# Kernel tuning notes

Measured on AMD Instinct MI355X. Metric: run time of the kernel, lower is better.

## Reference

```python
import jax, jax.numpy as jnp
import numpy as np

KH = KW = 3
C_IN = 3
FILTERS = 32
STRIDE = 2
LN_EPS = 1e-3  # keras LayerNormalization default


def _conv(inp, k, strides):
    return jax.lax.conv_general_dilated(
        inp, k, window_strides=strides, padding='SAME',
        dimension_numbers=('NHWC', 'HWIO', 'NHWC'))


def _hard_sigmoid(z):
    # keras hard_sigmoid: 0.2*x + 0.5, clipped to [0, 1]
    return jnp.clip(z * 0.2 + 0.5, 0.0, 1.0)


def setup_inputs() -> dict:
    key = jax.random.key(0)
    ks = jax.random.split(key, 6)
    B, T, H, W = 16, 24, 112, 112
    F = FILTERS
    Hp, Wp = H // STRIDE, W // STRIDE
    D = Hp * Wp * F
    x = jax.random.normal(ks[0], (B, T, H, W, C_IN), dtype=jnp.float32)
    Wk = jax.random.normal(ks[1], (KH, KW, C_IN, 4 * F), dtype=jnp.float32) * 0.05
    Uk = jax.random.normal(ks[2], (KH, KW, F, 4 * F), dtype=jnp.float32) * 0.05
    b = jax.random.normal(ks[3], (4 * F,), dtype=jnp.float32) * 0.05
    gamma = jnp.ones((D,), dtype=jnp.float32)
    beta = jnp.zeros((D,), dtype=jnp.float32)
    return {'x': x, 'Wk': Wk, 'Uk': Uk, 'b': b, 'gamma': gamma, 'beta': beta}


def reference(x, Wk, Uk, b, gamma, beta):
    B, T, H, W, C = x.shape
    F = Uk.shape[2]
    # Input-to-gate convs are time-independent: batch them over B*T in one conv.
    xg = _conv(x.reshape(B * T, H, W, C), Wk, (STRIDE, STRIDE)) + b
    Hp, Wp = xg.shape[1], xg.shape[2]
    xg = xg.reshape(B, T, Hp, Wp, 4 * F).transpose(1, 0, 2, 3, 4)  # (T,B,Hp,Wp,4F)

    def step(carry, xt):
        h, c = carry
        z = xt + _conv(h, Uk, (1, 1))
        zi, zf, zc, zo = jnp.split(z, 4, axis=-1)
        i = _hard_sigmoid(zi)
        f = _hard_sigmoid(zf)
        o = _hard_sigmoid(zo)
        c_new = f * c + i * jnp.tanh(zc)
        h_new = o * jnp.tanh(c_new)
        return (h_new, c_new), h_new

    h0 = jnp.zeros((B, Hp, Wp, F), x.dtype)
    _, hs = jax.lax.scan(step, (h0, h0), xg)  # hs: (T,B,Hp,Wp,F)

    y = hs.transpose(1, 0, 2, 3, 4).reshape(B, T, Hp * Wp * F)
    mu = jnp.mean(y, axis=-1, keepdims=True)
    var = jnp.mean(jnp.square(y - mu), axis=-1, keepdims=True)
    yn = (y - mu) * jax.lax.rsqrt(var + LN_EPS)
    return yn * gamma + beta
```

## Files before the change

kernel.cpp:

```cpp
#include <hip/hip_runtime.h>
#include <math.h>

#define NB 16
#define NT 24
#define HP 56
#define WP 56
#define NF 32
#define ND (HP*WP*NF)
#define NHPQ 14
#define HPITCH 36
#define LN_EPS 1e-3f

typedef __attribute__((ext_vector_type(8))) short short8;
typedef __attribute__((ext_vector_type(4))) float floatx4;

#define AT_LD(p)     __hip_atomic_load((p), __ATOMIC_RELAXED, __HIP_MEMORY_SCOPE_AGENT)
#define AT_ST(p, v)  __hip_atomic_store((p), (v), __ATOMIC_RELAXED, __HIP_MEMORY_SCOPE_AGENT)
#define AT_ADD(p, v) __hip_atomic_fetch_add((p), (v), __ATOMIC_RELAXED, __HIP_MEMORY_SCOPE_AGENT)

__device__ __forceinline__ float tanh_fast(float x){
    float e = __expf(2.0f*x);
    return 1.0f - 2.0f*__builtin_amdgcn_rcpf(e + 1.0f);
}
__device__ __forceinline__ float hsig(float z){
    return fminf(fmaxf(z*0.2f + 0.5f, 0.0f), 1.0f);
}
__device__ __forceinline__ ushort f2bf(float v){
    unsigned u = __float_as_uint(v);
    return (ushort)((u + 0x7fffu + ((u >> 16) & 1u)) >> 16);
}

__global__ __launch_bounds__(512, 2)
void convlstm_persist(const float* __restrict__ x,
                      const float* __restrict__ Wk,
                      const float* __restrict__ Uk,
                      const float* __restrict__ bias,
                      const float* __restrict__ gamma,
                      const float* __restrict__ beta,
                      ushort* __restrict__ hbuf0,
                      ushort* __restrict__ hbuf1,
                      float* __restrict__ out,
                      float* __restrict__ stats,
                      int* __restrict__ cnt,
                      int* __restrict__ flags)
{
    __shared__ __attribute__((aligned(16))) ushort h_lds[6*66*HPITCH];
    __shared__ __attribute__((aligned(16))) ushort x_lds[9*344];
    __shared__ __attribute__((aligned(16))) ushort u_lds[9*128*32];
    __shared__ __attribute__((aligned(16))) ushort wk_lds[128*32];
    __shared__ float bcast[2];
    __shared__ float sred[8][2];

    const int tid  = threadIdx.x;
    const int hpq  = blockIdx.x;
    const int b    = blockIdx.y;
    const int lane = tid & 63;
    const int w    = tid >> 6;
    const int row  = w >> 1;
    const int fh   = w & 1;
    const int col  = lane & 15;
    const int q    = lane >> 4;
    const int q8   = q * 8;
    const int hp_g = hpq*4 + row;

    for (int e = tid; e < 6*66*HPITCH; e += 512) h_lds[e] = 0;
    for (int e = tid; e < 9*344;       e += 512) x_lds[e] = 0;
    for (int e = tid; e < 9*32*128; e += 512){
        int tap = e >> 12, k = (e >> 7) & 31, n = e & 127;
        u_lds[(tap*128 + n)*32 + k] = f2bf(Uk[e]);
    }
    for (int e = tid; e < 128*32; e += 512){
        int n = e >> 5, k = e & 31;
        wk_lds[e] = (k < 27) ? f2bf(Wk[k*128 + n]) : (ushort)0;
    }

    float bg[4];
    #pragma unroll
    for (int g = 0; g < 4; g++) bg[g] = bias[g*32 + fh*16 + col];

    float gr[4][4], br[4][4], creg[4][4], hreg[4][4];
    #pragma unroll
    for (int mt = 0; mt < 4; mt++)
      #pragma unroll
      for (int reg = 0; reg < 4; reg++){
          int wp = mt*16 + q*4 + reg;
          creg[mt][reg] = 0.f;
          hreg[mt][reg] = 0.f;
          if (wp < WP){
              size_t idx = (size_t)(hp_g*WP + wp)*NF + fh*16 + col;
              gr[mt][reg] = gamma[idx];
              br[mt][reg] = beta[idx];
          } else { gr[mt][reg] = 0.f; br[mt][reg] = 0.f; }
      }

    __syncthreads();

    for (int t = 0; t < NT; ++t){
        {
            const float* xt = x + ((size_t)(b*NT + t))*(112*112*3);
            for (int e = tid; e < 9*84; e += 512){
                int rrow = e / 84;
                int c4   = e - rrow*84;
                int rg   = 8*hpq + rrow;
                if (rg < 112){
                    float4 v = *(const float4*)&xt[rg*336 + c4*4];
                    ushort4 s4 = {f2bf(v.x), f2bf(v.y), f2bf(v.z), f2bf(v.w)};
                    *(ushort4*)&x_lds[rrow*344 + c4*4] = s4;
                }
            }
        }
        if (t > 0 && tid == 0){
            const int fb = ((t-1)*NB + b)*NHPQ;
            if (hpq > 0)
                while (AT_LD(&flags[fb + hpq-1]) == 0) __builtin_amdgcn_s_sleep(4);
            if (hpq < NHPQ-1)
                while (AT_LD(&flags[fb + hpq+1]) == 0) __builtin_amdgcn_s_sleep(4);
            asm volatile("" ::: "memory");
        }
        __syncthreads();

        uint4 hv = {0u,0u,0u,0u};
        int hoff = -1;
        if (t > 0 && tid < 448){
            const ushort* hsrc = ((t & 1) ? hbuf0 : hbuf1) + (size_t)b*ND;
            int rsel = (tid >= 224);
            int rem  = tid - rsel*224;
            int cg   = rem >> 2, cq = rem & 3;
            int rg   = rsel ? (hpq*4 + 4) : (hpq*4 - 1);
            int ldr  = rsel ? 5 : 0;
            if (rg >= 0 && rg < HP){
                const uint* sp = (const uint*)&hsrc[((size_t)rg*WP + cg)*NF + cq*8];
                hv.x = AT_LD(sp + 0);
                hv.y = AT_LD(sp + 1);
                hv.z = AT_LD(sp + 2);
                hv.w = AT_LD(sp + 3);
                hoff = (ldr*66 + 1 + cg)*HPITCH + cq*8;
            }
        }

        floatx4 acc[4][4];
        #pragma unroll
        for (int g = 0; g < 4; g++){
            floatx4 bv = (floatx4){bg[g], bg[g], bg[g], bg[g]};
            #pragma unroll
            for (int mt = 0; mt < 4; mt++) acc[mt][g] = bv;
        }

        {
            short8 ax[4];
            #pragma unroll
            for (int mt = 0; mt < 4; mt++){
                int wp = mt*16 + col;
                short8 v;
                #pragma unroll
                for (int j = 0; j < 8; j++){
                    int k = q8 + j;
                    ushort bits = 0;
                    if (k < 27){
                        int dy = k/9; int rr = k - dy*9; int dx = rr/3; int cc = rr - dx*3;
                        int xc = 2*wp + dx; if (xc > 112) xc = 112;
                        bits = x_lds[(2*row + dy)*344 + xc*3 + cc];
                    }
                    v[j] = (short)bits;
                }
                ax[mt] = v;
            }
            #pragma unroll
            for (int g = 0; g < 4; g++){
                short8 bx = *(const short8*)&wk_lds[(g*32 + fh*16 + col)*32 + q8];
                #pragma unroll
                for (int mt = 0; mt < 4; mt++)
                    acc[mt][g] = __builtin_amdgcn_mfma_f32_16x16x32_bf16(ax[mt], bx, acc[mt][g], 0, 0, 0);
            }
        }

        if (hoff >= 0) *(uint4*)&h_lds[hoff] = hv;
        __syncthreads();

        if (t > 0){
            #pragma unroll
            for (int tap = 0; tap < 9; tap++){
                int dy = tap/3, dx = tap - dy*3;
                short8 a_[4], bb_[4];
                #pragma unroll
                for (int g = 0; g < 4; g++)
                    bb_[g] = *(const short8*)&u_lds[(tap*128 + g*32 + fh*16 + col)*32 + q8];
                #pragma unroll
                for (int mt = 0; mt < 4; mt++)
                    a_[mt] = *(const short8*)&h_lds[((row + dy)*66 + mt*16 + col + dx)*HPITCH + q8];
                #pragma unroll
                for (int mt = 0; mt < 4; mt++)
                    #pragma unroll
                    for (int g = 0; g < 4; g++)
                        acc[mt][g] = __builtin_amdgcn_mfma_f32_16x16x32_bf16(a_[mt], bb_[g], acc[mt][g], 0, 0, 0);
            }
        }
        __syncthreads();

        if (t > 0){
            if (tid == 0){
                while (AT_LD(&cnt[b*NT + t-1]) < NHPQ) __builtin_amdgcn_s_sleep(4);
                asm volatile("" ::: "memory");
                float s  = AT_LD(&stats[(size_t)(b*NT + t-1)*2]);
                float ss = AT_LD(&stats[(size_t)(b*NT + t-1)*2 + 1]);
                float m  = s * (1.0f/(float)ND);
                float v  = ss * (1.0f/(float)ND) - m*m;
                bcast[0] = m;
                bcast[1] = rsqrtf(v + LN_EPS);
            }
            __syncthreads();
            const float mu = bcast[0], rs = bcast[1];
            float* orow = out + ((size_t)(b*NT + t - 1))*ND;
            #pragma unroll
            for (int mt = 0; mt < 4; mt++)
              #pragma unroll
              for (int reg = 0; reg < 4; reg++){
                  int wp = mt*16 + q*4 + reg;
                  if (wp < WP)
                      orow[(size_t)(hp_g*WP + wp)*NF + fh*16 + col] =
                          (hreg[mt][reg] - mu)*rs*gr[mt][reg] + br[mt][reg];
              }
        }

        float lsum = 0.f, lss = 0.f;
        #pragma unroll
        for (int mt = 0; mt < 4; mt++)
          #pragma unroll
          for (int reg = 0; reg < 4; reg++){
              int wp = mt*16 + q*4 + reg;
              float zi = acc[mt][0][reg];
              float zf = acc[mt][1][reg];
              float zc = acc[mt][2][reg];
              float zo = acc[mt][3][reg];
              float ig = hsig(zi), fg = hsig(zf), og = hsig(zo);
              float cn = fg*creg[mt][reg] + ig*tanh_fast(zc);
              float hv2 = og*tanh_fast(cn);
              if (wp < WP){
                  creg[mt][reg] = cn;
                  hreg[mt][reg] = hv2;
                  h_lds[((row + 1)*66 + 1 + wp)*HPITCH + fh*16 + col] = f2bf(hv2);
                  lsum += hv2;
                  lss  += hv2*hv2;
              }
          }

        if (row == 0 || row == 3){
            ushort* hdst = ((t & 1) ? hbuf1 : hbuf0) + (size_t)b*ND;
            int rg  = hpq*4 + row;
            int ldr = row ? 4 : 1;
            for (int e = lane; e < 112; e += 64){
                int cg = e >> 1, hf = e & 1;
                uint4 v = *(const uint4*)&h_lds[(ldr*66 + 1 + cg)*HPITCH + fh*16 + hf*8];
                uint* dp = (uint*)&hdst[((size_t)rg*WP + cg)*NF + fh*16 + hf*8];
                AT_ST(dp + 0, v.x);
                AT_ST(dp + 1, v.y);
                AT_ST(dp + 2, v.z);
                AT_ST(dp + 3, v.w);
            }
        }

        #pragma unroll
        for (int off = 32; off > 0; off >>= 1){
            lsum += __shfl_down(lsum, off);
            lss  += __shfl_down(lss, off);
        }
        if (lane == 0){ sred[w][0] = lsum; sred[w][1] = lss; }

        asm volatile("s_waitcnt vmcnt(0)" ::: "memory");
        __syncthreads();
        if (tid == 0){
            float a0 = 0.f, a1 = 0.f;
            #pragma unroll
            for (int i = 0; i < 8; i++){ a0 += sred[i][0]; a1 += sred[i][1]; }
            AT_ADD(&stats[(size_t)(b*NT + t)*2],     a0);
            AT_ADD(&stats[(size_t)(b*NT + t)*2 + 1], a1);
            asm volatile("s_waitcnt vmcnt(0)" ::: "memory");
            AT_ADD(&cnt[b*NT + t], 1);
            AT_ADD(&flags[((size_t)t*NB + b)*NHPQ + hpq], 1);
        }
    }

    if (tid == 0){
        while (AT_LD(&cnt[b*NT + NT-1]) < NHPQ) __builtin_amdgcn_s_sleep(4);
        asm volatile("" ::: "memory");
        float s  = AT_LD(&stats[(size_t)(b*NT + NT-1)*2]);
        float ss = AT_LD(&stats[(size_t)(b*NT + NT-1)*2 + 1]);
        float m  = s * (1.0f/(float)ND);
        float v  = ss * (1.0f/(float)ND) - m*m;
        bcast[0] = m;
        bcast[1] = rsqrtf(v + LN_EPS);
    }
    __syncthreads();
    {
        const float mu = bcast[0], rs = bcast[1];
        float* orow = out + ((size_t)(b*NT + NT - 1))*ND;
        #pragma unroll
        for (int mt = 0; mt < 4; mt++)
          #pragma unroll
          for (int reg = 0; reg < 4; reg++){
              int wp = mt*16 + q*4 + reg;
              if (wp < WP)
                  orow[(size_t)(hp_g*WP + wp)*NF + fh*16 + col] =
                      (hreg[mt][reg] - mu)*rs*gr[mt][reg] + br[mt][reg];
          }
    }
}

extern "C" void kernel_launch(void* const* d_in, const int* in_sizes, int n_in,
                              void* d_out, int out_size, void* d_ws, size_t ws_size,
                              hipStream_t stream)
{
    const float* x     = (const float*)d_in[0];
    const float* Wk    = (const float*)d_in[1];
    const float* Uk    = (const float*)d_in[2];
    const float* bias  = (const float*)d_in[3];
    const float* gamma = (const float*)d_in[4];
    const float* beta  = (const float*)d_in[5];
    float* out = (float*)d_out;

    char* p = (char*)d_ws;
    ushort* hbuf0 = (ushort*)p; p += (size_t)NB*ND*2;
    ushort* hbuf1 = (ushort*)p; p += (size_t)NB*ND*2;
    float*  stats = (float*)p;  p += (size_t)NB*NT*2*4;
    int*    cnt   = (int*)p;    p += (size_t)NB*NT*4;
    int*    flags = (int*)p;

    hipMemsetAsync(stats, 0, (size_t)(NB*NT*2*4 + NB*NT*4 + NT*NB*NHPQ*4), stream);
    hipLaunchKernelGGL(convlstm_persist, dim3(NHPQ, NB), dim3(512), 0, stream,
                       x, Wk, Uk, bias, gamma, beta,
                       hbuf0, hbuf1, out, stats, cnt, flags);
}
```

Baseline: 571.3 us.

## Defer LayerNorm output by two steps and signal halo flags earlier

The LayerNorm write-out for each timestep is delayed by two steps, so the global stats wait overlaps with an extra step of recurrence. This keeps two generations of h in registers and raises register pressure. Halo-ready flags are now raised once the boundary-row warps finish their global stores, instead of after the full block reduction, using an LDS counter. The change also pads the weight LDS layout to pitch 36 to reduce bank conflicts and shortens the spin-wait sleep.

```diff
diff --git a/kernel.cpp b/kernel.cpp
--- a/kernel.cpp
+++ b/kernel.cpp
@@ -9,6 +9,7 @@
 #define ND (HP*WP*NF)
 #define NHPQ 14
 #define HPITCH 36
+#define UPITCH 36
 #define LN_EPS 1e-3f
 
 typedef __attribute__((ext_vector_type(8))) short short8;
@@ -46,10 +47,11 @@
 {
     __shared__ __attribute__((aligned(16))) ushort h_lds[6*66*HPITCH];
     __shared__ __attribute__((aligned(16))) ushort x_lds[9*344];
-    __shared__ __attribute__((aligned(16))) ushort u_lds[9*128*32];
-    __shared__ __attribute__((aligned(16))) ushort wk_lds[128*32];
-    __shared__ float bcast[2];
+    __shared__ __attribute__((aligned(16))) ushort u_lds[9*128*UPITCH];
+    __shared__ __attribute__((aligned(16))) ushort wk_lds[128*UPITCH];
+    __shared__ float bcast4[4];
     __shared__ float sred[8][2];
+    __shared__ int   ecnt[NT];
 
     const int tid  = threadIdx.x;
     const int hpq  = blockIdx.x;
@@ -67,25 +69,25 @@
     for (int e = tid; e < 9*344;       e += 512) x_lds[e] = 0;
     for (int e = tid; e < 9*32*128; e += 512){
         int tap = e >> 12, k = (e >> 7) & 31, n = e & 127;
-        u_lds[(tap*128 + n)*32 + k] = f2bf(Uk[e]);
+        u_lds[(tap*128 + n)*UPITCH + k] = f2bf(Uk[e]);
     }
     for (int e = tid; e < 128*32; e += 512){
         int n = e >> 5, k = e & 31;
-        wk_lds[e] = (k < 27) ? f2bf(Wk[k*128 + n]) : (ushort)0;
-    }
+        wk_lds[n*UPITCH + k] = (k < 27) ? f2bf(Wk[k*128 + n]) : (ushort)0;
+    }
+    for (int e = tid; e < NT; e += 512) ecnt[e] = 0;
 
     float bg[4];
     #pragma unroll
     for (int g = 0; g < 4; g++) bg[g] = bias[g*32 + fh*16 + col];
 
-    float gr[4][4], br[4][4], creg[4][4], hreg[4][4];
+    float gr[4][4], br[4][4], creg[4][4], hregA[4][4], hregB[4][4];
     #pragma unroll
     for (int mt = 0; mt < 4; mt++)
       #pragma unroll
       for (int reg = 0; reg < 4; reg++){
           int wp = mt*16 + q*4 + reg;
-          creg[mt][reg] = 0.f;
-          hreg[mt][reg] = 0.f;
+          creg[mt][reg] = 0.f; hregA[mt][reg] = 0.f; hregB[mt][reg] = 0.f;
           if (wp < WP){
               size_t idx = (size_t)(hp_g*WP + wp)*NF + fh*16 + col;
               gr[mt][reg] = gamma[idx];
@@ -112,9 +114,9 @@
         if (t > 0 && tid == 0){
             const int fb = ((t-1)*NB + b)*NHPQ;
             if (hpq > 0)
-                while (AT_LD(&flags[fb + hpq-1]) == 0) __builtin_amdgcn_s_sleep(4);
+                while (AT_LD(&flags[fb + hpq-1]) == 0) __builtin_amdgcn_s_sleep(1);
             if (hpq < NHPQ-1)
-                while (AT_LD(&flags[fb + hpq+1]) == 0) __builtin_amdgcn_s_sleep(4);
+                while (AT_LD(&flags[fb + hpq+1]) == 0) __builtin_amdgcn_s_sleep(1);
             asm volatile("" ::: "memory");
         }
         __syncthreads();
@@ -167,7 +169,7 @@
             }
             #pragma unroll
             for (int g = 0; g < 4; g++){
-                short8 bx = *(const short8*)&wk_lds[(g*32 + fh*16 + col)*32 + q8];
+                short8 bx = *(const short8*)&wk_lds[(g*32 + fh*16 + col)*UPITCH + q8];
                 #pragma unroll
                 for (int mt = 0; mt < 4; mt++)
                     acc[mt][g] = __builtin_amdgcn_mfma_f32_16x16x32_bf16(ax[mt], bx, acc[mt][g], 0, 0, 0);
@@ -184,7 +186,7 @@
                 short8 a_[4], bb_[4];
                 #pragma unroll
                 for (int g = 0; g < 4; g++)
-                    bb_[g] = *(const short8*)&u_lds[(tap*128 + g*32 + fh*16 + col)*32 + q8];
+                    bb_[g] = *(const short8*)&u_lds[(tap*128 + g*32 + fh*16 + col)*UPITCH + q8];
                 #pragma unroll
                 for (int mt = 0; mt < 4; mt++)
                     a_[mt] = *(const short8*)&h_lds[((row + dy)*66 + mt*16 + col + dx)*HPITCH + q8];
@@ -197,31 +199,7 @@
         }
         __syncthreads();
 
-        if (t > 0){
-            if (tid == 0){
-                while (AT_LD(&cnt[b*NT + t-1]) < NHPQ) __builtin_amdgcn_s_sleep(4);
-                asm volatile("" ::: "memory");
-                float s  = AT_LD(&stats[(size_t)(b*NT + t-1)*2]);
-                float ss = AT_LD(&stats[(size_t)(b*NT + t-1)*2 + 1]);
-                float m  = s * (1.0f/(float)ND);
-                float v  = ss * (1.0f/(float)ND) - m*m;
-                bcast[0] = m;
-                bcast[1] = rsqrtf(v + LN_EPS);
-            }
-            __syncthreads();
-            const float mu = bcast[0], rs = bcast[1];
-            float* orow = out + ((size_t)(b*NT + t - 1))*ND;
-            #pragma unroll
-            for (int mt = 0; mt < 4; mt++)
-              #pragma unroll
-              for (int reg = 0; reg < 4; reg++){
-                  int wp = mt*16 + q*4 + reg;
-                  if (wp < WP)
-                      orow[(size_t)(hp_g*WP + wp)*NF + fh*16 + col] =
-                          (hreg[mt][reg] - mu)*rs*gr[mt][reg] + br[mt][reg];
-              }
-        }
-
+        float hnew[4][4];
         float lsum = 0.f, lss = 0.f;
         #pragma unroll
         for (int mt = 0; mt < 4; mt++)
@@ -235,9 +213,10 @@
               float ig = hsig(zi), fg = hsig(zf), og = hsig(zo);
               float cn = fg*creg[mt][reg] + ig*tanh_fast(zc);
               float hv2 = og*tanh_fast(cn);
+              hnew[mt][reg] = 0.f;
               if (wp < WP){
                   creg[mt][reg] = cn;
-                  hreg[mt][reg] = hv2;
+                  hnew[mt][reg] = hv2;
                   h_lds[((row + 1)*66 + 1 + wp)*HPITCH + fh*16 + col] = f2bf(hv2);
                   lsum += hv2;
                   lss  += hv2*hv2;
@@ -257,6 +236,11 @@
                 AT_ST(dp + 2, v.z);
                 AT_ST(dp + 3, v.w);
             }
+            asm volatile("s_waitcnt vmcnt(0)" ::: "memory");
+            if (lane == 0){
+                if (atomicAdd(&ecnt[t], 1) == 3)
+                    AT_ADD(&flags[((size_t)t*NB + b)*NHPQ + hpq], 1);
+            }
         }
 
         #pragma unroll
@@ -266,8 +250,18 @@
         }
         if (lane == 0){ sred[w][0] = lsum; sred[w][1] = lss; }
 
-        asm volatile("s_waitcnt vmcnt(0)" ::: "memory");
+        if (t >= 2 && tid == 128){
+            while (AT_LD(&cnt[b*NT + t-2]) < NHPQ) __builtin_amdgcn_s_sleep(1);
+            asm volatile("" ::: "memory");
+            float s  = AT_LD(&stats[(size_t)(b*NT + t-2)*2]);
+            float ss = AT_LD(&stats[(size_t)(b*NT + t-2)*2 + 1]);
+            float m  = s * (1.0f/(float)ND);
+            float vv = ss * (1.0f/(float)ND) - m*m;
+            bcast4[0] = m;
+            bcast4[1] = rsqrtf(vv + LN_EPS);
+        }
         __syncthreads();
+
         if (tid == 0){
             float a0 = 0.f, a1 = 0.f;
             #pragma unroll
@@ -276,24 +270,53 @@
             AT_ADD(&stats[(size_t)(b*NT + t)*2 + 1], a1);
             asm volatile("s_waitcnt vmcnt(0)" ::: "memory");
             AT_ADD(&cnt[b*NT + t], 1);
-            AT_ADD(&flags[((size_t)t*NB + b)*NHPQ + hpq], 1);
-        }
-    }
-
-    if (tid == 0){
-        while (AT_LD(&cnt[b*NT + NT-1]) < NHPQ) __builtin_amdgcn_s_sleep(4);
+        }
+
+        if (t >= 2){
+            const float mu = bcast4[0], rs = bcast4[1];
+            float* orow = out + ((size_t)(b*NT + t - 2))*ND;
+            #pragma unroll
+            for (int mt = 0; mt < 4; mt++)
+              #pragma unroll
+              for (int reg = 0; reg < 4; reg++){
+                  int wp = mt*16 + q*4 + reg;
+                  if (wp < WP)
+                      orow[(size_t)(hp_g*WP + wp)*NF + fh*16 + col] =
+                          (hregB[mt][reg] - mu)*rs*gr[mt][reg] + br[mt][reg];
+              }
+        }
+
+        #pragma unroll
+        for (int mt = 0; mt < 4; mt++)
+          #pragma unroll
+          for (int reg = 0; reg < 4; reg++){
+              hregB[mt][reg] = hregA[mt][reg];
+              hregA[mt][reg] = hnew[mt][reg];
+          }
+    }
+
+    if (tid == 128){
+        while (AT_LD(&cnt[b*NT + NT-2]) < NHPQ) __builtin_amdgcn_s_sleep(1);
         asm volatile("" ::: "memory");
-        float s  = AT_LD(&stats[(size_t)(b*NT + NT-1)*2]);
-        float ss = AT_LD(&stats[(size_t)(b*NT + NT-1)*2 + 1]);
+        float s  = AT_LD(&stats[(size_t)(b*NT + NT-2)*2]);
+        float ss = AT_LD(&stats[(size_t)(b*NT + NT-2)*2 + 1]);
         float m  = s * (1.0f/(float)ND);
-        float v  = ss * (1.0f/(float)ND) - m*m;
-        bcast[0] = m;
-        bcast[1] = rsqrtf(v + LN_EPS);
+        float vv = ss * (1.0f/(float)ND) - m*m;
+        bcast4[0] = m;
+        bcast4[1] = rsqrtf(vv + LN_EPS);
+        while (AT_LD(&cnt[b*NT + NT-1]) < NHPQ) __builtin_amdgcn_s_sleep(1);
+        asm volatile("" ::: "memory");
+        s  = AT_LD(&stats[(size_t)(b*NT + NT-1)*2]);
+        ss = AT_LD(&stats[(size_t)(b*NT + NT-1)*2 + 1]);
+        m  = s * (1.0f/(float)ND);
+        vv = ss * (1.0f/(float)ND) - m*m;
+        bcast4[2] = m;
+        bcast4[3] = rsqrtf(vv + LN_EPS);
     }
     __syncthreads();
     {
-        const float mu = bcast[0], rs = bcast[1];
-        float* orow = out + ((size_t)(b*NT + NT - 1))*ND;
+        float mu = bcast4[0], rs = bcast4[1];
+        float* orow = out + ((size_t)(b*NT + NT - 2))*ND;
         #pragma unroll
         for (int mt = 0; mt < 4; mt++)
           #pragma unroll
@@ -301,7 +324,18 @@
               int wp = mt*16 + q*4 + reg;
               if (wp < WP)
                   orow[(size_t)(hp_g*WP + wp)*NF + fh*16 + col] =
-                      (hreg[mt][reg] - mu)*rs*gr[mt][reg] + br[mt][reg];
+                      (hregB[mt][reg] - mu)*rs*gr[mt][reg] + br[mt][reg];
+          }
+        mu = bcast4[2]; rs = bcast4[3];
+        orow = out + ((size_t)(b*NT + NT - 1))*ND;
+        #pragma unroll
+        for (int mt = 0; mt < 4; mt++)
+          #pragma unroll
+          for (int reg = 0; reg < 4; reg++){
+              int wp = mt*16 + q*4 + reg;
+              if (wp < WP)
+                  orow[(size_t)(hp_g*WP + wp)*NF + fh*16 + col] =
+                      (hregA[mt][reg] - mu)*rs*gr[mt][reg] + br[mt][reg];
           }
     }
 }
```

Measured after the change: 730.5 us. +27.9%, slower.
